# Kernel optimization log

Measured on AMD Instinct MI355X. Metric: run time of the kernel, lower is better.

## Reference

```python
import jax, jax.numpy as jnp
import numpy as np
from jax import lax

EPOCHS = 3
N_IN, N_OUT = 20, 18
BN_EPS = 1e-5
RECT_EPS = 1e-4
TRIU = np.triu_indices(N_OUT)  # SPDVectorize upper-triangular indices


def _orth(key, n, m):
    # Stiefel init: orthonormal columns, like nn.init.orthogonal_
    q, _ = jnp.linalg.qr(jax.random.normal(key, (n, m), dtype=jnp.float32))
    return q


def setup_inputs() -> dict:
    key = jax.random.key(0)
    ks = jax.random.split(key, 8)
    bs = 2048
    f32 = jnp.float32
    return dict(
        x=jax.random.normal(ks[0], (bs, 1, 22, 438), dtype=f32),
        W1=jax.random.normal(ks[1], (22, 1, 22, 1), dtype=f32) * 0.1,
        b1=jnp.zeros((22,), f32),
        g1=jnp.ones((22,), f32), be1=jnp.zeros((22,), f32),
        W2=jax.random.normal(ks[2], (20, 22, 1, 12), dtype=f32) * 0.05,
        b2=jnp.zeros((20,), f32),
        g2=jnp.ones((20,), f32), be2=jnp.zeros((20,), f32),
        Wq=_orth(ks[3], N_IN, N_OUT),
        Wk=_orth(ks[4], N_IN, N_OUT),
        Wv=_orth(ks[5], N_IN, N_OUT),
        Wl=jax.random.normal(ks[6], (N_OUT * (N_OUT + 1) // 2 * EPOCHS, 4), dtype=f32) * 0.02,
        bl=jnp.zeros((4,), f32),
    )


def _bn(x, g, b):
    # BatchNorm2d forward in training mode (batch statistics, biased var)
    mean = x.mean(axis=(0, 2, 3), keepdims=True)
    var = ((x - mean) ** 2).mean(axis=(0, 2, 3), keepdims=True)
    return (x - mean) * lax.rsqrt(var + BN_EPS) * g[None, :, None, None] + b[None, :, None, None]


def _conv(x, w, b, pad_w):
    y = lax.conv_general_dilated(x, w, (1, 1), [(0, 0), (pad_w, pad_w)],
                                 dimension_numbers=('NCHW', 'OIHW', 'NCHW'))
    return y + b[None, :, None, None]


def _signal2spd(x):
    # x: (bs, C, L) -> trace-normalized covariance + 1e-5 * I
    L = x.shape[-1]
    xc = x - x.mean(-1, keepdims=True)
    cov = jnp.einsum('bcl,bdl->bcd', xc, xc) / (L - 1)
    cov = cov / jnp.trace(cov, axis1=-2, axis2=-1)[:, None, None]
    return cov + 1e-5 * jnp.eye(cov.shape[-1], dtype=cov.dtype)


def _patch_lens(n, epochs):
    base = n // epochs
    lens = [base] * epochs
    for i in range(n - base * epochs):
        lens[i] += 1
    return lens


def _spd_fn(t, fn):
    # SPD functional calculus via eigh (== torch.svd on SPD input)
    s, u = jnp.linalg.eigh(t)
    return jnp.einsum('...ij,...j,...kj->...ik', u, fn(s), u)


def _forward(x, W1, b1, g1, be1, W2, b2, g2, be2, Wq, Wk, Wv, Wl, bl):
    bs = x.shape[0]
    h = _bn(_conv(x, W1, b1, 0), g1, be1)          # (bs,22,1,438)
    h = _bn(_conv(h, W2, b2, 6), g2, be2)          # (bs,20,1,439)
    sig = h[:, :, 0, :]                            # squeeze -> (bs,20,439)
    covs, off = [], 0
    for L in _patch_lens(sig.shape[-1], EPOCHS):   # E2R: [147,146,146]
        covs.append(_signal2spd(sig[:, :, off:off + L]))
        off += L
    X = jnp.stack(covs, axis=1)                    # (bs,m,20,20) SPD
    # SPDTransform: W^T X W with Stiefel W (20,18)
    Q = jnp.einsum('pi,bmpq,qj->bmij', Wq, X, Wq)
    K = jnp.einsum('pi,bmpq,qj->bmij', Wk, X, Wk)
    V = jnp.einsum('pi,bmpq,qj->bmij', Wv, X, Wv)
    logQ = _spd_fn(Q, jnp.log)
    logK = _spd_fn(K, jnp.log)
    logV = _spd_fn(V, jnp.log)
    # log-Euclidean distance^2: ||log Q_j - log K_i||_F^2  (== sum of svd singvals of D D^T)
    diff = logQ[:, :, None] - logK[:, None, :]     # (bs, mq, mk, n, n)
    energy = jnp.sum(diff * diff, axis=(-2, -1))   # (bs, mq, mk)
    scores = 1.0 / (1.0 + jnp.log1p(energy))
    # torch: softmax over dim=-2 then permute(0,2,1) == softmax over K index here
    P = jax.nn.softmax(scores, axis=-1)            # (bs, mq, mk)
    mixed = jnp.einsum('bji,bipq->bjpq', P, logV)  # weighted log-Euclidean mean
    out = _spd_fn(mixed, jnp.exp)
    out = _spd_fn(out, lambda s: jnp.maximum(s, RECT_EPS))  # SPDRectified
    logO = _spd_fn(out, jnp.log)                   # SPDTangentSpace log
    vec = logO[..., TRIU[0], TRIU[1]]              # (bs, m, 171)
    return vec.reshape(bs, -1) @ Wl + bl           # (bs, 4)


def reference(x, W1, b1, g1, be1, W2, b2, g2, be2, Wq, Wk, Wv, Wl, bl):
    return _forward(x, W1, b1, g1, be1, W2, b2, g2, be2, Wq, Wk, Wv, Wl, bl)
```

## Files before the change

kernel.cpp:

```cpp
#include <hip/hip_runtime.h>
#include <math.h>

#define OFF_Y2   0
#define OFF_QKV  17981440
#define OFF_ST   (17981440 + 5971968)
#define ST_SX   0
#define ST_SXX  22
#define ST_WF   506
#define ST_BF   990
#define ST_Y2S  1012
#define ST_Y2Q  1032
#define ST_TOT  1052

#define LOGEPS -9.210340371976182f
#define NSWEEP 5
#define SHIFT  12.0f

__global__ __launch_bounds__(256) void k0_zero(float* __restrict__ st){
  for (int i = threadIdx.x; i < ST_TOT; i += 256) st[i] = 0.f;
}

__global__ __launch_bounds__(256) void k1_xstats(const float* __restrict__ x, float* __restrict__ st){
  __shared__ __align__(16) float xs[22*444];
  const float* xb = x + (size_t)blockIdx.x * (22*438);
  for (int i = threadIdx.x; i < 22*444; i += 256){
    int h = i / 444, w = i - h*444;
    xs[i] = (w < 438) ? xb[h*438 + w] : 0.f;
  }
  __syncthreads();
  for (int t = threadIdx.x; t < 275; t += 256){
    if (t < 22){
      const float4* r = (const float4*)&xs[t*444];
      float4 acc = {0.f,0.f,0.f,0.f};
      for (int w = 0; w < 111; ++w){ float4 v = r[w]; acc.x+=v.x; acc.y+=v.y; acc.z+=v.z; acc.w+=v.w; }
      atomicAdd(&st[ST_SX + t], acc.x+acc.y+acc.z+acc.w);
    } else {
      int rem = t - 22, h = 0;
      while (rem >= 22 - h){ rem -= 22 - h; ++h; }
      int h2 = h + rem;
      const float4* ra = (const float4*)&xs[h*444];
      const float4* rb = (const float4*)&xs[h2*444];
      float4 acc = {0.f,0.f,0.f,0.f};
      for (int w = 0; w < 111; ++w){
        float4 a = ra[w], b = rb[w];
        acc.x = fmaf(a.x,b.x,acc.x); acc.y = fmaf(a.y,b.y,acc.y);
        acc.z = fmaf(a.z,b.z,acc.z); acc.w = fmaf(a.w,b.w,acc.w);
      }
      atomicAdd(&st[ST_SXX + h*22 + h2], acc.x+acc.y+acc.z+acc.w);
    }
  }
}

__global__ __launch_bounds__(64) void k1b_fold(const float* __restrict__ W1, const float* __restrict__ g1,
                                               const float* __restrict__ be1, float* __restrict__ st){
  int c = threadIdx.x;
  if (c >= 22) return;
  const float invN = 1.f / (2048.f*438.f);
  float mcol[22];
  float mu0 = 0.f;
  for (int h = 0; h < 22; ++h){ mcol[h] = W1[c*22 + h]; mu0 = fmaf(mcol[h], st[ST_SX + h], mu0); }
  mu0 *= invN;
  float qf = 0.f;
  for (int h = 0; h < 22; ++h)
    for (int h2 = h; h2 < 22; ++h2){
      float w = mcol[h]*mcol[h2]*st[ST_SXX + h*22 + h2];
      qf += (h2 == h) ? w : 2.f*w;
    }
  qf *= invN;
  float var = qf - mu0*mu0;
  float a1 = g1[c] * rsqrtf(var + 1e-5f);
  for (int h = 0; h < 22; ++h) st[ST_WF + h*22 + c] = a1 * mcol[h];
  st[ST_BF + c] = be1[c] - a1 * mu0;
}

__global__ __launch_bounds__(256, 3) void k3_conv(const float* __restrict__ x, const float* __restrict__ W2,
                                                  float* __restrict__ st, float* __restrict__ y2){
  __shared__ __align__(16) float zs[22*452 + 20];
  __shared__ __align__(16) float w2s[10*268];
  __shared__ __align__(16) float wfs[22*24];
  __shared__ float bfs[22];
  __shared__ float sloc[10], qloc[10];
  int tid = threadIdx.x;
  int n = blockIdx.x;
  int dbase = blockIdx.y * 10;
  for (int i = tid; i < 484; i += 256){ int h = i/22, c = i - h*22; wfs[h*24 + c] = st[ST_WF + i]; }
  for (int i = tid; i < 2640; i += 256){ int dl = i/264, r = i - dl*264; w2s[dl*268 + r] = W2[(dbase + dl)*264 + r]; }
  if (tid < 22) bfs[tid] = st[ST_BF + tid];
  if (tid < 10){ sloc[tid] = 0.f; qloc[tid] = 0.f; }
  for (int i = tid; i < 22*14; i += 256){ int c = i/14, k = i - c*14; int w = (k < 6) ? k : (438 + k); zs[c*452 + w] = 0.f; }
  __syncthreads();
  if (tid < 219){
    float2 acc[22];
    #pragma unroll
    for (int c = 0; c < 22; ++c){ float b = bfs[c]; acc[c].x = b; acc[c].y = b; }
    const float* xb = x + (size_t)n*(22*438) + 2*tid;
    #pragma unroll 1
    for (int h = 0; h < 22; ++h){
      float2 xv = *(const float2*)&xb[h*438];
      #pragma unroll
      for (int c = 0; c < 22; ++c){
        float w = wfs[h*24 + c];
        acc[c].x = fmaf(w, xv.x, acc[c].x);
        acc[c].y = fmaf(w, xv.y, acc[c].y);
      }
    }
    #pragma unroll
    for (int c = 0; c < 22; ++c) *(float2*)&zs[c*452 + 6 + 2*tid] = acc[c];
  }
  __syncthreads();
  if (tid < 190){
    int chunk = tid / 10, dl = tid - chunk*10;
    int d = dbase + dl;
    int w0 = chunk*24;
    float acc[24];
    #pragma unroll
    for (int jj = 0; jj < 24; ++jj) acc[jj] = 0.f;
    #pragma unroll 1
    for (int c = 0; c < 22; ++c){
      const float* zr = &zs[c*452 + w0];
      float zw[36];
      #pragma unroll
      for (int k = 0; k < 36; k += 4){ float4 v = *(const float4*)&zr[k]; zw[k]=v.x; zw[k+1]=v.y; zw[k+2]=v.z; zw[k+3]=v.w; }
      const float* wr = &w2s[dl*268 + c*12];
      float wt[12];
      #pragma unroll
      for (int t = 0; t < 12; t += 4){ float4 v = *(const float4*)&wr[t]; wt[t]=v.x; wt[t+1]=v.y; wt[t+2]=v.z; wt[t+3]=v.w; }
      #pragma unroll
      for (int jj = 0; jj < 24; ++jj)
        #pragma unroll
        for (int t = 0; t < 12; ++t)
          acc[jj] = fmaf(wt[t], zw[jj+t], acc[jj]);
    }
    float* yb = y2 + (size_t)n*8780 + d*439;
    float s = 0.f, q = 0.f;
    #pragma unroll
    for (int jj = 0; jj < 24; ++jj){
      int w = w0 + jj;
      if (w < 439){ yb[w] = acc[jj]; s += acc[jj]; q = fmaf(acc[jj], acc[jj], q); }
    }
    atomicAdd(&sloc[dl], s);
    atomicAdd(&qloc[dl], q);
  }
  __syncthreads();
  if (tid < 10){
    atomicAdd(&st[ST_Y2S + dbase + tid], sloc[tid]);
    atomicAdd(&st[ST_Y2Q + dbase + tid], qloc[tid]);
  }
}

__global__ __launch_bounds__(256) void k4_cov_qkv(const float* __restrict__ y2, const float* __restrict__ st,
    const float* __restrict__ g2, const float* __restrict__ Wq, const float* __restrict__ Wk,
    const float* __restrict__ Wv, float* __restrict__ qkv){
  __shared__ __align__(16) float ysp[3][20][148];
  __shared__ float a2s[20];
  __shared__ __align__(16) float Bt[3][18][20];
  __shared__ __align__(16) float G3[3][400];
  __shared__ __align__(16) float Tmt[3][360];
  __shared__ float musum3[3][20];
  __shared__ float rtr3[3];
  int tid = threadIdx.x, n = blockIdx.x;
  if (tid < 20){
    const float invN = 1.f/(2048.f*439.f);
    float s = st[ST_Y2S + tid]*invN;
    float q = st[ST_Y2Q + tid]*invN;
    a2s[tid] = g2[tid] * rsqrtf(q - s*s + 1e-5f);
  }
  const float* yb = y2 + (size_t)n*8780;
  for (int i = tid; i < 8780; i += 256){
    int d = i/439, w = i - d*439;
    int m = (w >= 293) ? 2 : ((w >= 147) ? 1 : 0);
    int lw = w - ((m == 2) ? 293 : ((m == 1) ? 147 : 0));
    ysp[m][d][lw] = yb[i];
  }
  if (tid < 100){
    int d = tid/5, k = tid - d*5;
    int m = (k == 0) ? 0 : ((k < 3) ? 1 : 2);
    int lw = (k == 0) ? 147 : ((k == 1 || k == 3) ? 146 : 147);
    ysp[m][d][lw] = 0.f;
  }
  __syncthreads();
  for (int i = tid; i < 1140; i += 256){
    if (i < 1080){
      int wt = i/360, r = i - wt*360; int d = r/18, jj = r - d*18;
      const float* Wm = (wt==0) ? Wq : ((wt==1) ? Wk : Wv);
      Bt[wt][jj][d] = a2s[d]*Wm[d*18 + jj];
    } else {
      int t = i - 1080; int m = t/20, d = t - m*20;
      const float4* r = (const float4*)&ysp[m][d][0];
      float4 acc = {0.f,0.f,0.f,0.f};
      #pragma unroll 1
      for (int w = 0; w < 37; ++w){ float4 v = r[w]; acc.x+=v.x; acc.y+=v.y; acc.z+=v.z; acc.w+=v.w; }
      musum3[m][d] = acc.x+acc.y+acc.z+acc.w;
    }
  }
  __syncthreads();
  for (int it = tid; it < 630; it += 256){
    int m = it/210, t = it - m*210;
    int rem = t, c = 0;
    while (rem >= 20 - c){ rem -= 20 - c; ++c; }
    int d = c + rem;
    const float4* ra = (const float4*)&ysp[m][c][0];
    const float4* rb = (const float4*)&ysp[m][d][0];
    float4 acc4 = {0.f,0.f,0.f,0.f};
    #pragma unroll 1
    for (int w = 0; w < 37; ++w){
      float4 a = ra[w], b = rb[w];
      acc4.x = fmaf(a.x,b.x,acc4.x); acc4.y = fmaf(a.y,b.y,acc4.y);
      acc4.z = fmaf(a.z,b.z,acc4.z); acc4.w = fmaf(a.w,b.w,acc4.w);
    }
    float invL = (m == 0) ? (1.f/147.f) : (1.f/146.f);
    float acc = (acc4.x+acc4.y+acc4.z+acc4.w) - musum3[m][c]*musum3[m][d]*invL;
    G3[m][c*20 + d] = acc; G3[m][d*20 + c] = acc;
  }
  __syncthreads();
  for (int wt = 0; wt < 3; ++wt){
    for (int i = tid; i < 1083; i += 256){
      if (i < 1080){
        int m = i/360, r = i - m*360; int p = r/18, jj = r - p*18;
        const float4* gr = (const float4*)&G3[m][p*20];
        const float4* br = (const float4*)&Bt[wt][jj][0];
        float4 a4 = {0.f,0.f,0.f,0.f};
        #pragma unroll
        for (int w = 0; w < 5; ++w){
          float4 a = gr[w], b = br[w];
          a4.x = fmaf(a.x,b.x,a4.x); a4.y = fmaf(a.y,b.y,a4.y);
          a4.z = fmaf(a.z,b.z,a4.z); a4.w = fmaf(a.w,b.w,a4.w);
        }
        Tmt[m][jj*20 + p] = a4.x+a4.y+a4.z+a4.w;
      } else if (wt == 0){
        int m = i - 1080;
        float tr = 0.f;
        for (int c = 0; c < 20; ++c){ float a = a2s[c]; tr = fmaf(a*a, G3[m][c*21], tr); }
        rtr3[m] = 1.f/tr;
      }
    }
    __syncthreads();
    for (int it = tid; it < 513; it += 256){
      int m = it/171, t = it - m*171;
      int rem = t, i = 0;
      while (rem >= 18 - i){ rem -= 18 - i; ++i; }
      int jj = i + rem;
      const float4* br = (const float4*)&Bt[wt][i][0];
      const float4* tr = (const float4*)&Tmt[m][jj*20];
      float4 a4 = {0.f,0.f,0.f,0.f};
      #pragma unroll
      for (int w = 0; w < 5; ++w){
        float4 a = br[w], b = tr[w];
        a4.x = fmaf(a.x,b.x,a4.x); a4.y = fmaf(a.y,b.y,a4.y);
        a4.z = fmaf(a.z,b.z,a4.z); a4.w = fmaf(a.w,b.w,a4.w);
      }
      float acc = (a4.x+a4.y+a4.z+a4.w) * rtr3[m];
      if (i == jj) acc += 1e-5f;
      float* outm = qkv + ((size_t)wt*6144 + (size_t)n*3 + m)*324;
      outm[i*18 + jj] = acc; outm[jj*18 + i] = acc;
    }
    __syncthreads();
  }
}

__global__ __launch_bounds__(256, 4) void k5_oneside(const float* __restrict__ src, float* __restrict__ dst,
    int nmat, int mode, const float* __restrict__ Wl, const float* __restrict__ bl,
    float* __restrict__ outp){
  __shared__ __align__(16) float stage[12][384];
  __shared__ __align__(16) float wls[2052];
  __shared__ float outacc[4][4];
  int tid = threadIdx.x;
  int wave = tid >> 6, lane = tid & 63;
  int g = (lane >= 54) ? 3 : (lane >= 36 ? 2 : (lane >= 18 ? 1 : 0));
  int j = lane - g*18;
  int gb = g*18;
  int slot = wave*3 + ((g < 3) ? g : 0);
  int mat = blockIdx.x*12 + wave*3 + g;
  bool act = (g < 3) && (mat < nmat);

  if (mode == 1){
    for (int i = tid; i < 2052; i += 256) wls[i] = Wl[i];
    if (tid < 16) outacc[tid >> 2][tid & 3] = 0.f;
  }

  float b[18];
  float sh = (mode == 1) ? SHIFT : 0.f;
  if (act){
    const float* s = src + (size_t)mat*324 + j*18;
    #pragma unroll
    for (int i = 0; i < 18; ++i) b[i] = s[i] + ((i == j) ? sh : 0.f);
  } else {
    #pragma unroll
    for (int i = 0; i < 18; ++i) b[i] = (i == j) ? 1.f : 0.f;
  }
  float nrm;
  { float n0 = 0.f, n1 = 0.f;
    #pragma unroll
    for (int k = 0; k < 18; k += 2){ n0 = fmaf(b[k],b[k],n0); n1 = fmaf(b[k+1],b[k+1],n1); }
    nrm = n0 + n1; }

  #pragma unroll 1
  for (int sweep = 0; sweep < NSWEEP; ++sweep){
    #pragma unroll
    for (int r = 0; r < 17; ++r){
      int xx = j - 1 - r; if (xx < 0) xx += 17;
      int v = r + 17 - xx; if (v >= 17) v -= 17;
      int m = (j == 0) ? (1 + r) : ((xx == 0) ? 0 : (1 + v));
      bool isp = (j == 0) ? true : ((xx == 0) ? false : (xx <= 8));
      int plane = (gb + m) & 63;
      float rv[18];
      #pragma unroll
      for (int k = 0; k < 18; ++k) rv[k] = __shfl(b[k], plane);
      float on = __shfl(nrm, plane);
      float g0 = 0.f, g1 = 0.f;
      #pragma unroll
      for (int k = 0; k < 18; k += 2){ g0 = fmaf(b[k], rv[k], g0); g1 = fmaf(b[k+1], rv[k+1], g1); }
      float gam = g0 + g1;
      float alpha = isp ? nrm : on;
      float beta  = isp ? on  : nrm;
      float tau = (beta - alpha) * 0.5f * __builtin_amdgcn_rcpf(gam);
      float tt = __builtin_amdgcn_rcpf(fabsf(tau) + sqrtf(fmaf(tau, tau, 1.f)));
      float t = (tau >= 0.f) ? tt : -tt;
      if (!(fabsf(gam) > 1e-36f)) t = 0.f;
      float c = __builtin_amdgcn_rsqf(fmaf(t, t, 1.f));
      float s = t*c;
      nrm = fmaf(isp ? -t : t, gam, nrm);
      float sg = isp ? -s : s;
      #pragma unroll
      for (int k = 0; k < 18; ++k) b[k] = fmaf(c, b[k], sg*rv[k]);
    }
  }
  float n0 = 0.f, n1 = 0.f;
  #pragma unroll
  for (int k = 0; k < 18; k += 2){ n0 = fmaf(b[k],b[k],n0); n1 = fmaf(b[k+1],b[k+1],n1); }
  float nf = fmaxf(n0 + n1, 1e-30f);
  float fv = (mode == 0) ? (0.5f * logf(nf)) : fmaxf(sqrtf(nf) - SHIFT, LOGEPS);
  float wv = fv * __builtin_amdgcn_rcpf(nf);
  float* sp = &stage[slot][0];
  if (act){
    #pragma unroll
    for (int k = 0; k < 18; ++k) sp[k*20 + j] = b[k];
    sp[360 + j] = wv;
  }
  __syncthreads();
  if (act){
    float wr[18];
    #pragma unroll
    for (int i = 0; i < 18; ++i) wr[i] = sp[j*20 + i] * sp[360 + i];
    float frow[18];
    #pragma unroll
    for (int i2 = 0; i2 < 18; ++i2){
      const float* br = &sp[i2*20];
      float a0 = 0.f;
      #pragma unroll
      for (int k = 0; k < 16; k += 4){
        float4 v4 = *(const float4*)&br[k];
        a0 = fmaf(wr[k],   v4.x, a0); a0 = fmaf(wr[k+1], v4.y, a0);
        a0 = fmaf(wr[k+2], v4.z, a0); a0 = fmaf(wr[k+3], v4.w, a0);
      }
      a0 = fmaf(wr[16], br[16], a0);
      a0 = fmaf(wr[17], br[17], a0);
      frow[i2] = a0;
    }
    if (mode == 0){
      float* orow = dst + (size_t)mat*324 + j*18;
      #pragma unroll
      for (int i2 = 0; i2 < 18; ++i2) orow[i2] = frow[i2];
    } else {
      int base = (g*171 + j*(37 - j)/2 - j)*4;
      float o0=0.f, o1=0.f, o2=0.f, o3=0.f;
      #pragma unroll
      for (int jj = 0; jj < 18; ++jj){
        if (jj >= j){
          const float* w4 = &wls[base + jj*4];
          o0 = fmaf(frow[jj], w4[0], o0);
          o1 = fmaf(frow[jj], w4[1], o1);
          o2 = fmaf(frow[jj], w4[2], o2);
          o3 = fmaf(frow[jj], w4[3], o3);
        }
      }
      atomicAdd(&outacc[wave][0], o0);
      atomicAdd(&outacc[wave][1], o1);
      atomicAdd(&outacc[wave][2], o2);
      atomicAdd(&outacc[wave][3], o3);
    }
  }
  if (mode == 1){
    __syncthreads();
    if (tid < 16){
      int bi = tid >> 2, o = tid & 3;
      outp[(blockIdx.x*4 + bi)*4 + o] = outacc[bi][o] + bl[o];
    }
  }
}

__global__ __launch_bounds__(128) void k6_attnmix(const float* __restrict__ logs, float* __restrict__ mixed){
  __shared__ float lq[972], lk[972], lv[972];
  __shared__ float ew[2][9];
  __shared__ float P[9];
  int b = blockIdx.x, tid = threadIdx.x;
  const float* q  = logs + (size_t)b*972;
  const float* k_ = logs + 1990656 + (size_t)b*972;
  const float* v_ = logs + 3981312 + (size_t)b*972;
  for (int i = tid; i < 972; i += 128){ lq[i] = q[i]; lk[i] = k_[i]; lv[i] = v_[i]; }
  __syncthreads();
  float e[9] = {0.f,0.f,0.f,0.f,0.f,0.f,0.f,0.f,0.f};
  for (int x = tid; x < 324; x += 128){
    float q0 = lq[x], q1 = lq[324+x], q2 = lq[648+x];
    float k0 = lk[x], k1 = lk[324+x], k2 = lk[648+x];
    float d;
    d = q0-k0; e[0] = fmaf(d,d,e[0]);
    d = q0-k1; e[1] = fmaf(d,d,e[1]);
    d = q0-k2; e[2] = fmaf(d,d,e[2]);
    d = q1-k0; e[3] = fmaf(d,d,e[3]);
    d = q1-k1; e[4] = fmaf(d,d,e[4]);
    d = q1-k2; e[5] = fmaf(d,d,e[5]);
    d = q2-k0; e[6] = fmaf(d,d,e[6]);
    d = q2-k1; e[7] = fmaf(d,d,e[7]);
    d = q2-k2; e[8] = fmaf(d,d,e[8]);
  }
  #pragma unroll
  for (int p = 0; p < 9; ++p)
    for (int off = 32; off; off >>= 1) e[p] += __shfl_down(e[p], off);
  if ((tid & 63) == 0){
    #pragma unroll
    for (int p = 0; p < 9; ++p) ew[tid >> 6][p] = e[p];
  }
  __syncthreads();
  if (tid < 3){
    float en0 = ew[0][tid*3+0] + ew[1][tid*3+0];
    float en1 = ew[0][tid*3+1] + ew[1][tid*3+1];
    float en2 = ew[0][tid*3+2] + ew[1][tid*3+2];
    float s0 = 1.f/(1.f + log1pf(en0));
    float s1 = 1.f/(1.f + log1pf(en1));
    float s2 = 1.f/(1.f + log1pf(en2));
    float mx = fmaxf(s0, fmaxf(s1, s2));
    float e0 = expf(s0-mx), e1 = expf(s1-mx), e2 = expf(s2-mx);
    float inv = 1.f/(e0+e1+e2);
    P[tid*3+0] = e0*inv; P[tid*3+1] = e1*inv; P[tid*3+2] = e2*inv;
  }
  __syncthreads();
  float p00=P[0],p01=P[1],p02=P[2],p10=P[3],p11=P[4],p12=P[5],p20=P[6],p21=P[7],p22=P[8];
  float* mb = mixed + (size_t)b*972;
  for (int x = tid; x < 324; x += 128){
    float v0 = lv[x], v1 = lv[324+x], v2 = lv[648+x];
    mb[x]     = p00*v0 + p01*v1 + p02*v2;
    mb[324+x] = p10*v0 + p11*v1 + p12*v2;
    mb[648+x] = p20*v0 + p21*v1 + p22*v2;
  }
}

extern "C" void kernel_launch(void* const* d_in, const int* in_sizes, int n_in,
                              void* d_out, int out_size, void* d_ws, size_t ws_size,
                              hipStream_t stream){
  (void)in_sizes; (void)n_in; (void)out_size; (void)ws_size;
  const float* x   = (const float*)d_in[0];
  const float* W1  = (const float*)d_in[1];
  const float* g1  = (const float*)d_in[3];
  const float* be1 = (const float*)d_in[4];
  const float* W2  = (const float*)d_in[5];
  const float* g2  = (const float*)d_in[7];
  const float* Wq  = (const float*)d_in[9];
  const float* Wk  = (const float*)d_in[10];
  const float* Wv  = (const float*)d_in[11];
  const float* Wl  = (const float*)d_in[12];
  const float* bl  = (const float*)d_in[13];
  float* ws    = (float*)d_ws;
  float* y2    = ws + OFF_Y2;
  float* qkv   = ws + OFF_QKV;
  float* logs  = ws + OFF_Y2;
  float* mixed = ws + OFF_QKV;
  float* st    = ws + OFF_ST;
  float* outp  = (float*)d_out;

  k0_zero    <<<dim3(1),       dim3(256), 0, stream>>>(st);
  k1_xstats  <<<dim3(2048),    dim3(256), 0, stream>>>(x, st);
  k1b_fold   <<<dim3(1),       dim3(64),  0, stream>>>(W1, g1, be1, st);
  k3_conv    <<<dim3(2048,2),  dim3(256), 0, stream>>>(x, W2, st, y2);
  k4_cov_qkv <<<dim3(2048),    dim3(256), 0, stream>>>(y2, st, g2, Wq, Wk, Wv, qkv);
  k5_oneside <<<dim3(1536),    dim3(256), 0, stream>>>(qkv, logs, 18432, 0, nullptr, nullptr, nullptr);
  k6_attnmix <<<dim3(2048),    dim3(128), 0, stream>>>(logs, mixed);
  k5_oneside <<<dim3(512),     dim3(256), 0, stream>>>(mixed, nullptr, 6144, 1, Wl, bl, outp);
}
```

Before: 745.6 us.

## Fold BN1-conv1 into conv2 weights and apply conv2 directly to input

Adds a small kernel that precomputes effective conv2 weights by composing the folded BN1/conv1 matrix with W2, plus prefix sums of the bias contribution used to correct the zero-padded edges. The conv kernel then convolves the raw input directly, which removes the intermediate 22-channel z stage and its shared-memory staging. It also retiles the work into four blocks per sample, each covering half the width and half the output channels, with a smaller shared footprint and higher occupancy. The trade-offs are an extra serial single-block launch, some input re-reads from the width halo, and reuse of the qkv workspace region for the weights.

Result: slower. 788.8 us (+5.8%).

```diff
diff --git a/kernel.cpp b/kernel.cpp
--- a/kernel.cpp
+++ b/kernel.cpp
@@ -73,70 +73,90 @@
   st[ST_BF + c] = be1[c] - a1 * mu0;
 }
 
-__global__ __launch_bounds__(256, 3) void k3_conv(const float* __restrict__ x, const float* __restrict__ W2,
-                                                  float* __restrict__ st, float* __restrict__ y2){
-  __shared__ __align__(16) float zs[22*452 + 20];
-  __shared__ __align__(16) float w2s[10*268];
-  __shared__ __align__(16) float wfs[22*24];
-  __shared__ float bfs[22];
+__global__ __launch_bounds__(256) void k2_weff(const float* __restrict__ W2, const float* __restrict__ st,
+                                               float* __restrict__ weff, float* __restrict__ pfx){
+  __shared__ float wf[484];
+  __shared__ float bf[22];
+  for (int i = threadIdx.x; i < 484; i += 256) wf[i] = st[ST_WF + i];
+  if (threadIdx.x < 22) bf[threadIdx.x] = st[ST_BF + threadIdx.x];
+  __syncthreads();
+  for (int i = threadIdx.x; i < 5280; i += 256){
+    int d = i / 264, r = i - d*264, h = r / 12, t = r - h*12;
+    float a = 0.f;
+    for (int c = 0; c < 22; ++c) a = fmaf(W2[d*264 + c*12 + t], wf[h*22 + c], a);
+    weff[i] = a;
+  }
+  if (threadIdx.x < 20){
+    int d = threadIdx.x;
+    float run = 0.f;
+    pfx[d*13 + 0] = 0.f;
+    for (int t = 0; t < 12; ++t){
+      float a = 0.f;
+      for (int c = 0; c < 22; ++c) a = fmaf(W2[d*264 + c*12 + t], bf[c], a);
+      run += a;
+      pfx[d*13 + t + 1] = run;
+    }
+  }
+}
+
+__global__ __launch_bounds__(256, 5) void k3_conv(const float* __restrict__ x,
+    const float* __restrict__ weff, const float* __restrict__ pfx,
+    float* __restrict__ st, float* __restrict__ y2){
+  __shared__ __align__(16) float xs[22*236];
+  __shared__ __align__(16) float ws[10*264];
+  __shared__ float ps[130];
   __shared__ float sloc[10], qloc[10];
   int tid = threadIdx.x;
-  int n = blockIdx.x;
-  int dbase = blockIdx.y * 10;
-  for (int i = tid; i < 484; i += 256){ int h = i/22, c = i - h*22; wfs[h*24 + c] = st[ST_WF + i]; }
-  for (int i = tid; i < 2640; i += 256){ int dl = i/264, r = i - dl*264; w2s[dl*268 + r] = W2[(dbase + dl)*264 + r]; }
-  if (tid < 22) bfs[tid] = st[ST_BF + tid];
+  int dh = blockIdx.x & 1, wh = blockIdx.x >> 1;
+  int n = blockIdx.y;
+  int wbase = wh*220, dbase = dh*10;
+  const float* xb = x + (size_t)n*9636;
+  for (int i = tid; i < 22*232; i += 256){
+    int h = i / 232, lw = i - h*232;
+    int gw = wbase - 6 + lw;
+    xs[h*236 + lw] = (gw >= 0 && gw < 438) ? xb[h*438 + gw] : 0.f;
+  }
+  for (int i = tid; i < 2640; i += 256) ws[i] = weff[dbase*264 + i];
+  if (tid < 130) ps[tid] = pfx[dbase*13 + tid];
   if (tid < 10){ sloc[tid] = 0.f; qloc[tid] = 0.f; }
-  for (int i = tid; i < 22*14; i += 256){ int c = i/14, k = i - c*14; int w = (k < 6) ? k : (438 + k); zs[c*452 + w] = 0.f; }
-  __syncthreads();
-  if (tid < 219){
-    float2 acc[22];
-    #pragma unroll
-    for (int c = 0; c < 22; ++c){ float b = bfs[c]; acc[c].x = b; acc[c].y = b; }
-    const float* xb = x + (size_t)n*(22*438) + 2*tid;
+  __syncthreads();
+  if (tid < 220){
+    int dl = tid / 22, wc = tid - dl*22;
+    float acc[10];
+    #pragma unroll
+    for (int j = 0; j < 10; ++j) acc[j] = 0.f;
     #pragma unroll 1
     for (int h = 0; h < 22; ++h){
-      float2 xv = *(const float2*)&xb[h*438];
-      #pragma unroll
-      for (int c = 0; c < 22; ++c){
-        float w = wfs[h*24 + c];
-        acc[c].x = fmaf(w, xv.x, acc[c].x);
-        acc[c].y = fmaf(w, xv.y, acc[c].y);
+      const float* xr = &xs[h*236 + wc*10];
+      float xw[21];
+      #pragma unroll
+      for (int k = 0; k < 10; ++k) *(float2*)&xw[2*k] = *(const float2*)&xr[2*k];
+      xw[20] = xr[20];
+      const float* wr = &ws[dl*264 + h*12];
+      float wt[12];
+      #pragma unroll
+      for (int t = 0; t < 12; t += 4){ float4 v = *(const float4*)&wr[t]; wt[t]=v.x; wt[t+1]=v.y; wt[t+2]=v.z; wt[t+3]=v.w; }
+      #pragma unroll
+      for (int t = 0; t < 12; ++t)
+        #pragma unroll
+        for (int j = 0; j < 10; ++j)
+          acc[j] = fmaf(wt[t], xw[j+t], acc[j]);
+    }
+    int d = dbase + dl;
+    float* yb = y2 + (size_t)n*8780 + d*439;
+    const float* pr = &ps[dl*13];
+    float s = 0.f, q = 0.f;
+    int w0 = wbase + wc*10;
+    #pragma unroll
+    for (int j = 0; j < 10; ++j){
+      int gw = w0 + j;
+      if (gw < 439){
+        int lo = 6 - gw; lo = (lo > 0) ? lo : 0;
+        int hi = 444 - gw; hi = (hi < 12) ? hi : 12;
+        float val = acc[j] + pr[hi] - pr[lo];
+        yb[gw] = val;
+        s += val; q = fmaf(val, val, q);
       }
-    }
-    #pragma unroll
-    for (int c = 0; c < 22; ++c) *(float2*)&zs[c*452 + 6 + 2*tid] = acc[c];
-  }
-  __syncthreads();
-  if (tid < 190){
-    int chunk = tid / 10, dl = tid - chunk*10;
-    int d = dbase + dl;
-    int w0 = chunk*24;
-    float acc[24];
-    #pragma unroll
-    for (int jj = 0; jj < 24; ++jj) acc[jj] = 0.f;
-    #pragma unroll 1
-    for (int c = 0; c < 22; ++c){
-      const float* zr = &zs[c*452 + w0];
-      float zw[36];
-      #pragma unroll
-      for (int k = 0; k < 36; k += 4){ float4 v = *(const float4*)&zr[k]; zw[k]=v.x; zw[k+1]=v.y; zw[k+2]=v.z; zw[k+3]=v.w; }
-      const float* wr = &w2s[dl*268 + c*12];
-      float wt[12];
-      #pragma unroll
-      for (int t = 0; t < 12; t += 4){ float4 v = *(const float4*)&wr[t]; wt[t]=v.x; wt[t+1]=v.y; wt[t+2]=v.z; wt[t+3]=v.w; }
-      #pragma unroll
-      for (int jj = 0; jj < 24; ++jj)
-        #pragma unroll
-        for (int t = 0; t < 12; ++t)
-          acc[jj] = fmaf(wt[t], zw[jj+t], acc[jj]);
-    }
-    float* yb = y2 + (size_t)n*8780 + d*439;
-    float s = 0.f, q = 0.f;
-    #pragma unroll
-    for (int jj = 0; jj < 24; ++jj){
-      int w = w0 + jj;
-      if (w < 439){ yb[w] = acc[jj]; s += acc[jj]; q = fmaf(acc[jj], acc[jj], q); }
     }
     atomicAdd(&sloc[dl], s);
     atomicAdd(&qloc[dl], q);
@@ -463,6 +483,8 @@
   float* ws    = (float*)d_ws;
   float* y2    = ws + OFF_Y2;
   float* qkv   = ws + OFF_QKV;
+  float* weff  = ws + OFF_QKV;
+  float* pfx   = ws + OFF_QKV + 5280;
   float* logs  = ws + OFF_Y2;
   float* mixed = ws + OFF_QKV;
   float* st    = ws + OFF_ST;
@@ -471,7 +493,8 @@
   k0_zero    <<<dim3(1),       dim3(256), 0, stream>>>(st);
   k1_xstats  <<<dim3(2048),    dim3(256), 0, stream>>>(x, st);
   k1b_fold   <<<dim3(1),       dim3(64),  0, stream>>>(W1, g1, be1, st);
-  k3_conv    <<<dim3(2048,2),  dim3(256), 0, stream>>>(x, W2, st, y2);
+  k2_weff    <<<dim3(1),       dim3(256), 0, stream>>>(W2, st, weff, pfx);
+  k3_conv    <<<dim3(4,2048),  dim3(256), 0, stream>>>(x, weff, pfx, st, y2);
   k4_cov_qkv <<<dim3(2048),    dim3(256), 0, stream>>>(y2, st, g2, Wq, Wk, Wv, qkv);
   k5_oneside <<<dim3(1536),    dim3(256), 0, stream>>>(qkv, logs, 18432, 0, nullptr, nullptr, nullptr);
   k6_attnmix <<<dim3(2048),    dim3(128), 0, stream>>>(logs, mixed);
```
